# Kernel optimization log

Measured on AMD Instinct MI355X. Metric: run time of the kernel, lower is better.

The kernel has to match this reference:

```python
import jax, jax.numpy as jnp
import numpy as np

B, T, D_MODEL, N_HEADS = 2, 2048, 1024, 16


def setup_inputs() -> dict:
    key = jax.random.key(0)
    ks = jax.random.split(key, 5)
    w_scale = 0.02
    return {
        "x": jax.random.normal(ks[0], (B, T, D_MODEL), jnp.float32),
        "Wq": jax.random.normal(ks[1], (D_MODEL, D_MODEL), jnp.float32) * w_scale,
        "Wk": jax.random.normal(ks[2], (D_MODEL, D_MODEL), jnp.float32) * w_scale,
        "Wv": jax.random.normal(ks[3], (D_MODEL, D_MODEL), jnp.float32) * w_scale,
        "Wo": jax.random.normal(ks[4], (D_MODEL, D_MODEL), jnp.float32) * w_scale,
    }


def reference(x, Wq, Wk, Wv, Wo):
    Bv, Tv, _ = x.shape
    H = N_HEADS
    D = D_MODEL // H
    # Projections (torch nn.Linear: y = x @ W.T), split heads -> (B, H, T, D)
    q = (x @ Wq.T).reshape(Bv, Tv, H, D).transpose(0, 2, 1, 3)
    k = (x @ Wk.T).reshape(Bv, Tv, H, D).transpose(0, 2, 1, 3)
    v = (x @ Wv.T).reshape(Bv, Tv, H, D).transpose(0, 2, 1, 3)

    scale = jnp.sqrt(jnp.asarray(D, jnp.float32))
    scores = jnp.einsum("bhqd,bhkd->bhqk", q, k) / scale  # (B, H, T, T)

    # ALiBi bias: -|i-j| * slope_h, future positions masked to -inf (causal)
    slopes = jnp.asarray(
        [2.0 ** (-8.0 * h / H) for h in range(1, H + 1)], jnp.float32
    )
    pos = jnp.arange(Tv)
    dist = jnp.abs(pos[None, :] - pos[:, None]).astype(jnp.float32)  # (T, T)
    bias = -dist[None, :, :] * slopes[:, None, None]                 # (H, T, T)
    causal_mask = jnp.triu(jnp.ones((Tv, Tv), dtype=bool), 1)
    bias = jnp.where(causal_mask[None, :, :], -jnp.inf, bias)
    scores = scores + bias[None]  # (B, H, T, T)

    attn = jax.nn.softmax(scores, axis=-1)
    out = jnp.einsum("bhqk,bhkd->bhqd", attn, v)
    out = out.transpose(0, 2, 1, 3).reshape(Bv, Tv, D_MODEL)
    return out @ Wo.T
```

## Files before the change

kernel.cpp:

```cpp
#include <hip/hip_runtime.h>


#define DEV __device__ __forceinline__

typedef __attribute__((ext_vector_type(8))) short short8;
typedef __attribute__((ext_vector_type(4))) float f32x4;
typedef __attribute__((ext_vector_type(4))) unsigned short ushort4v;

DEV unsigned short f2bf(float f) {
  unsigned u = __builtin_bit_cast(unsigned, f);
  u += 0x7fffu + ((u >> 16) & 1u);
  return (unsigned short)(u >> 16);
}

DEV void gl2lds16(const void* g, void* l) {
  __builtin_amdgcn_global_load_lds(
      (const __attribute__((address_space(1))) void*)g,
      (__attribute__((address_space(3))) void*)l, 16, 0, 0);
}

__global__ __launch_bounds__(256) void cvt_all(
    const float* __restrict__ x, const float* __restrict__ wq,
    const float* __restrict__ wk, const float* __restrict__ wv,
    const float* __restrict__ wo, unsigned short* __restrict__ xb,
    unsigned short* __restrict__ wqb, unsigned short* __restrict__ wkb,
    unsigned short* __restrict__ wvb, unsigned short* __restrict__ wob) {
  int b = blockIdx.x;
  const float* s;
  unsigned short* d;
  int off;
  if (b < 4096)      { s = x;  d = xb;  off = b; }
  else if (b < 5120) { s = wq; d = wqb; off = b - 4096; }
  else if (b < 6144) { s = wk; d = wkb; off = b - 5120; }
  else if (b < 7168) { s = wv; d = wvb; off = b - 6144; }
  else               { s = wo; d = wob; off = b - 7168; }
  int i = (off * 256 + threadIdx.x) * 4;
  float4 v = *(const float4*)(s + i);
  ushort4v o = {f2bf(v.x), f2bf(v.y), f2bf(v.z), f2bf(v.w)};
  *(ushort4v*)(d + i) = o;
}

__global__ __launch_bounds__(256, 2) void gemm_qkv(
    const unsigned short* __restrict__ A, const unsigned short* __restrict__ Wq,
    const unsigned short* __restrict__ Wk, const unsigned short* __restrict__ Wv,
    unsigned short* __restrict__ Qo, unsigned short* __restrict__ Ko,
    unsigned short* __restrict__ Vo) {
  constexpr int K = 1024;
  __shared__ alignas(16) unsigned short Al[128 * 32];
  __shared__ alignas(16) unsigned short Bl[128 * 32];
  const int t = threadIdx.x;
  const int l = t & 63, l15 = l & 15, l4 = l >> 4;
  const int wm = ((t >> 6) & 1) * 64, wn = (t >> 7) * 64;
  const int wsel = blockIdx.x >> 3;
  const int n0 = (blockIdx.x & 7) * 128;
  const int m0 = blockIdx.y * 128;
  const unsigned short* Bm = (wsel == 0) ? Wq : ((wsel == 1) ? Wk : Wv);

  f32x4 zero4 = {0.f, 0.f, 0.f, 0.f};
  f32x4 acc[4][4];
#pragma unroll
  for (int i = 0; i < 4; i++)
#pragma unroll
    for (int j = 0; j < 4; j++) acc[i][j] = zero4;

  const int row0 = t >> 2, seg = (t & 3) * 8;
  const unsigned short* Ag0 = A + (m0 + row0) * K + seg;
  const unsigned short* Ag1 = A + (m0 + row0 + 64) * K + seg;
  const unsigned short* Bg0 = Bm + (n0 + row0) * K + seg;
  const unsigned short* Bg1 = Bm + (n0 + row0 + 64) * K + seg;

  for (int k0 = 0; k0 < K; k0 += 32) {
    gl2lds16(Ag0 + k0, &Al[t * 8]);
    gl2lds16(Ag1 + k0, &Al[2048 + t * 8]);
    gl2lds16(Bg0 + k0, &Bl[t * 8]);
    gl2lds16(Bg1 + k0, &Bl[2048 + t * 8]);
    __syncthreads();
    short8 af[4], bf8[4];
#pragma unroll
    for (int mi = 0; mi < 4; mi++)
      af[mi] = *(const short8*)&Al[(wm + mi * 16 + l15) * 32 + l4 * 8];
#pragma unroll
    for (int ni = 0; ni < 4; ni++)
      bf8[ni] = *(const short8*)&Bl[(wn + ni * 16 + l15) * 32 + l4 * 8];
#pragma unroll
    for (int mi = 0; mi < 4; mi++)
#pragma unroll
      for (int ni = 0; ni < 4; ni++)
        acc[mi][ni] = __builtin_amdgcn_mfma_f32_16x16x32_bf16(
            af[mi], bf8[ni], acc[mi][ni], 0, 0, 0);
    __syncthreads();
  }

  unsigned short* D = (wsel == 0) ? Qo : ((wsel == 1) ? Ko : Vo);
  const float scale = (wsel == 0) ? 0.18033688011112042f : 1.0f;
#pragma unroll
  for (int mi = 0; mi < 4; mi++)
#pragma unroll
    for (int r = 0; r < 4; r++) {
      int m = m0 + wm + mi * 16 + l4 * 4 + r;
      int b = m >> 11, tt = m & 2047;
#pragma unroll
      for (int ni = 0; ni < 4; ni++) {
        int n = n0 + wn + ni * 16 + l15;
        int z = b * 16 + (n >> 6), d = n & 63;
        float v = acc[mi][ni][r] * scale;
        int idx = (wsel == 2) ? ((z * 64 + d) * 2048 + tt)
                              : ((z * 2048 + tt) * 64 + d);
        D[idx] = f2bf(v);
      }
    }
}

__global__ __launch_bounds__(256, 2) void gemm_o(
    const unsigned short* __restrict__ A, const unsigned short* __restrict__ Bm,
    float* __restrict__ C) {
  constexpr int K = 1024;
  __shared__ alignas(16) unsigned short Al[128 * 32];
  __shared__ alignas(16) unsigned short Bl[128 * 32];
  const int t = threadIdx.x;
  const int l = t & 63, l15 = l & 15, l4 = l >> 4;
  const int wm = ((t >> 6) & 1) * 64, wn = (t >> 7) * 64;
  const int m0 = blockIdx.y * 128, n0 = blockIdx.x * 128;

  f32x4 zero4 = {0.f, 0.f, 0.f, 0.f};
  f32x4 acc[4][4];
#pragma unroll
  for (int i = 0; i < 4; i++)
#pragma unroll
    for (int j = 0; j < 4; j++) acc[i][j] = zero4;

  const int row0 = t >> 2, seg = (t & 3) * 8;
  const unsigned short* Ag0 = A + (m0 + row0) * K + seg;
  const unsigned short* Ag1 = A + (m0 + row0 + 64) * K + seg;
  const unsigned short* Bg0 = Bm + (n0 + row0) * K + seg;
  const unsigned short* Bg1 = Bm + (n0 + row0 + 64) * K + seg;

  for (int k0 = 0; k0 < K; k0 += 32) {
    gl2lds16(Ag0 + k0, &Al[t * 8]);
    gl2lds16(Ag1 + k0, &Al[2048 + t * 8]);
    gl2lds16(Bg0 + k0, &Bl[t * 8]);
    gl2lds16(Bg1 + k0, &Bl[2048 + t * 8]);
    __syncthreads();
    short8 af[4], bf8[4];
#pragma unroll
    for (int mi = 0; mi < 4; mi++)
      af[mi] = *(const short8*)&Al[(wm + mi * 16 + l15) * 32 + l4 * 8];
#pragma unroll
    for (int ni = 0; ni < 4; ni++)
      bf8[ni] = *(const short8*)&Bl[(wn + ni * 16 + l15) * 32 + l4 * 8];
#pragma unroll
    for (int mi = 0; mi < 4; mi++)
#pragma unroll
      for (int ni = 0; ni < 4; ni++)
        acc[mi][ni] = __builtin_amdgcn_mfma_f32_16x16x32_bf16(
            af[mi], bf8[ni], acc[mi][ni], 0, 0, 0);
    __syncthreads();
  }
#pragma unroll
  for (int mi = 0; mi < 4; mi++)
#pragma unroll
    for (int r = 0; r < 4; r++) {
      int m = m0 + wm + mi * 16 + l4 * 4 + r;
      float* cp = C + m * 1024 + n0 + wn + l15;
#pragma unroll
      for (int ni = 0; ni < 4; ni++) cp[ni * 16] = acc[mi][ni][r];
    }
}

__global__ __launch_bounds__(256, 3) void flash_alibi(
    const unsigned short* __restrict__ Q, const unsigned short* __restrict__ Kb,
    const unsigned short* __restrict__ Vt, unsigned short* __restrict__ O) {
  __shared__ alignas(16) unsigned short Kl[2 * 4096];
  __shared__ alignas(16) unsigned short Vl[2 * 4096];
  __shared__ alignas(16) unsigned short Pl[4 * 2304];
  const int t = threadIdx.x, w = t >> 6, l = t & 63, l15 = l & 15, l4 = l >> 4;
  const int g = blockIdx.x;
  const int qt = (g < 256) ? (15 - (g >> 5)) : ((g - 256) >> 5);
  const int z = g & 31;
  const int q0 = qt * 128, h = z & 15;
  const float slope2 = exp2f(-0.5f * (float)(h + 1)) * 1.4426950408889634f;
  const int qrow = q0 + w * 32;

  short8 aq[2][2];
#pragma unroll
  for (int mi = 0; mi < 2; mi++)
#pragma unroll
    for (int ks = 0; ks < 2; ks++)
      aq[mi][ks] = *(const short8*)&Q[(z * 2048 + qrow + mi * 16 + l15) * 64 +
                                      ks * 32 + l4 * 8];

  f32x4 binit[2];
#pragma unroll
  for (int mi = 0; mi < 2; mi++)
#pragma unroll
    for (int r = 0; r < 4; r++)
      binit[mi][r] =
          -(slope2 * (float)(qrow + mi * 16 + l4 * 4 + r) + 10.0f);

  f32x4 zero4 = {0.f, 0.f, 0.f, 0.f};
  f32x4 o[2][4];
  float lsum[2][4];
#pragma unroll
  for (int mi = 0; mi < 2; mi++)
#pragma unroll
    for (int j = 0; j < 4; j++) {
      o[mi][j] = zero4;
      lsum[mi][j] = 0.f;
    }

  const int row0 = t >> 2, seg8 = (t & 3) * 8;
  const int kvtiles = 2 * qt + 2;

#define ISSUE_LOADS(KV0, BUF)                                                \
  {                                                                          \
    unsigned short* Kd = &Kl[(BUF) * 4096];                                  \
    unsigned short* Vd = &Vl[(BUF) * 4096];                                  \
    gl2lds16(&Kb[(z * 2048 + (KV0) + row0) * 64 + seg8], &Kd[t * 8]);        \
    gl2lds16(&Kb[(z * 2048 + (KV0) + row0) * 64 + 32 + seg8],                \
             &Kd[2048 + t * 8]);                                             \
    gl2lds16(&Vt[(z * 64 + row0) * 2048 + (KV0) + seg8], &Vd[t * 8]);        \
    gl2lds16(&Vt[(z * 64 + row0) * 2048 + (KV0) + 32 + seg8],                \
             &Vd[2048 + t * 8]);                                             \
  }

  ISSUE_LOADS(0, 0)

  for (int it = 0; it < kvtiles; ++it) {
    __syncthreads();
    const int kv0 = it * 64;
    if (it + 1 < kvtiles) ISSUE_LOADS((it + 1) * 64, (it + 1) & 1)
    if (kv0 > qrow + 31) continue;
    const unsigned short* Kc = &Kl[(it & 1) * 4096];
    const unsigned short* Vc = &Vl[(it & 1) * 4096];

    f32x4 s[2][4];
#pragma unroll
    for (int mi = 0; mi < 2; mi++)
#pragma unroll
      for (int ni = 0; ni < 4; ni++) s[mi][ni] = binit[mi];
#pragma unroll
    for (int ks = 0; ks < 2; ks++) {
      short8 bk[4];
#pragma unroll
      for (int ni = 0; ni < 4; ni++)
        bk[ni] = *(const short8*)&Kc[(ks * 64 + ni * 16 + l15) * 32 + l4 * 8];
#pragma unroll
      for (int mi = 0; mi < 2; mi++)
#pragma unroll
        for (int ni = 0; ni < 4; ni++)
          s[mi][ni] = __builtin_amdgcn_mfma_f32_16x16x32_bf16(
              aq[mi][ks], bk[ni], s[mi][ni], 0, 0, 0);
    }

    const bool needMask = (kv0 + 63 > qrow);
    float jf[4];
#pragma unroll
    for (int ni = 0; ni < 4; ni++) jf[ni] = (float)(kv0 + ni * 16 + l15);

#pragma unroll
    for (int mi = 0; mi < 2; mi++)
#pragma unroll
      for (int r = 0; r < 4; r++) {
        float ps[4];
#pragma unroll
        for (int ni = 0; ni < 4; ni++)
          ps[ni] =
              __builtin_amdgcn_exp2f(fmaf(slope2, jf[ni], s[mi][ni][r]));
        if (needMask) {
          int qi = qrow + mi * 16 + l4 * 4 + r;
#pragma unroll
          for (int ni = 0; ni < 4; ni++)
            if (kv0 + ni * 16 + l15 > qi) ps[ni] = 0.f;
        }
        lsum[mi][r] += (ps[0] + ps[1]) + (ps[2] + ps[3]);
        int row = mi * 16 + l4 * 4 + r;
        unsigned short* pp = &Pl[w * 2304 + row * 72 + (l15 & 7)];
#pragma unroll
        for (int ni = 0; ni < 4; ni++)
          pp[((ni * 2 + (l15 >> 3)) ^ l4) * 8] = f2bf(ps[ni]);
      }

    asm volatile("s_waitcnt lgkmcnt(0)" ::: "memory");

    const int rsw = (l15 >> 2) & 3;
#pragma unroll
    for (int ks = 0; ks < 2; ks++) {
      short8 pf[2], vf[4];
#pragma unroll
      for (int mi = 0; mi < 2; mi++)
        pf[mi] = *(const short8*)&Pl[w * 2304 + (mi * 16 + l15) * 72 +
                                     ((ks * 4 + l4) ^ rsw) * 8];
#pragma unroll
      for (int nd = 0; nd < 4; nd++)
        vf[nd] = *(const short8*)&Vc[(ks * 64 + nd * 16 + l15) * 32 + l4 * 8];
#pragma unroll
      for (int mi = 0; mi < 2; mi++)
#pragma unroll
        for (int nd = 0; nd < 4; nd++)
          o[mi][nd] = __builtin_amdgcn_mfma_f32_16x16x32_bf16(
              pf[mi], vf[nd], o[mi][nd], 0, 0, 0);
    }
  }
#undef ISSUE_LOADS

  const int bq = z >> 4, hh = z & 15;
#pragma unroll
  for (int mi = 0; mi < 2; mi++)
#pragma unroll
    for (int r = 0; r < 4; r++) {
      float lv = lsum[mi][r];
#pragma unroll
      for (int off = 1; off < 16; off <<= 1) lv += __shfl_xor(lv, off);
      float inv = 1.0f / lv;
      int tg = qrow + mi * 16 + l4 * 4 + r;
      unsigned short* op = &O[(bq * 2048 + tg) * 1024 + hh * 64 + l15];
#pragma unroll
      for (int nd = 0; nd < 4; nd++) op[nd * 16] = f2bf(o[mi][nd][r] * inv);
    }
}

extern "C" void kernel_launch(void* const* d_in, const int* in_sizes, int n_in,
                              void* d_out, int out_size, void* d_ws,
                              size_t ws_size, hipStream_t stream) {
  const float* x = (const float*)d_in[0];
  const float* Wq = (const float*)d_in[1];
  const float* Wk = (const float*)d_in[2];
  const float* Wv = (const float*)d_in[3];
  const float* Wo = (const float*)d_in[4];

  char* p = (char*)d_ws;
  unsigned short* xb = (unsigned short*)p;  p += 4096 * 1024 * 2;
  unsigned short* wqb = (unsigned short*)p; p += 1024 * 1024 * 2;
  unsigned short* wkb = (unsigned short*)p; p += 1024 * 1024 * 2;
  unsigned short* wvb = (unsigned short*)p; p += 1024 * 1024 * 2;
  unsigned short* wob = (unsigned short*)p; p += 1024 * 1024 * 2;
  unsigned short* Qb = (unsigned short*)p;  p += 32 * 2048 * 64 * 2;
  unsigned short* Kbf = (unsigned short*)p; p += 32 * 2048 * 64 * 2;
  unsigned short* Vtb = (unsigned short*)p; p += 32 * 2048 * 64 * 2;
  unsigned short* Ob = (unsigned short*)p;  p += 4096 * 1024 * 2;

  cvt_all<<<8192, 256, 0, stream>>>(x, Wq, Wk, Wv, Wo, xb, wqb, wkb, wvb, wob);
  gemm_qkv<<<dim3(24, 32), 256, 0, stream>>>(xb, wqb, wkb, wvb, Qb, Kbf, Vtb);
  flash_alibi<<<512, 256, 0, stream>>>(Qb, Kbf, Vtb, Ob);
  gemm_o<<<dim3(8, 32), 256, 0, stream>>>(Ob, wob, (float*)d_out);
}
```

Baseline: 201.7 us.

## Split attention KV range across two blocks, add combine pass, retile output GEMM

The flash attention kernel now splits each query tile's KV range into two halves handled by separate blocks. Each block writes an unnormalized bf16 partial output and its row sums, and a new combine kernel adds the halves and normalizes. Because there is no running max, the two halves can be summed directly. The V transpose in the QKV GEMM is staged through shared memory so that global stores become coalesced 16-byte writes, and the output GEMM uses 128x64 tiles to double its block count. This is meant to improve load balance and occupancy on a part with many CUs, at the cost of an extra launch, extra intermediate traffic, and bf16 rounding of the partial sums.

Result: faster. 178.0 us (-11.7%).

```diff
diff --git a/kernel.cpp b/kernel.cpp
--- a/kernel.cpp
+++ b/kernel.cpp
@@ -11,6 +11,10 @@
   unsigned u = __builtin_bit_cast(unsigned, f);
   u += 0x7fffu + ((u >> 16) & 1u);
   return (unsigned short)(u >> 16);
+}
+DEV float bf2f(unsigned short u) {
+  unsigned x = ((unsigned)u) << 16;
+  return __builtin_bit_cast(float, x);
 }
 
 DEV void gl2lds16(const void* g, void* l) {
@@ -46,8 +50,9 @@
     unsigned short* __restrict__ Qo, unsigned short* __restrict__ Ko,
     unsigned short* __restrict__ Vo) {
   constexpr int K = 1024;
-  __shared__ alignas(16) unsigned short Al[128 * 32];
-  __shared__ alignas(16) unsigned short Bl[128 * 32];
+  __shared__ alignas(16) unsigned short Sm[18432];
+  unsigned short* Al = Sm;
+  unsigned short* Bl = Sm + 4096;
   const int t = threadIdx.x;
   const int l = t & 63, l15 = l & 15, l4 = l >> 4;
   const int wm = ((t >> 6) & 1) * 64, wn = (t >> 7) * 64;
@@ -91,24 +96,46 @@
     __syncthreads();
   }
 
-  unsigned short* D = (wsel == 0) ? Qo : ((wsel == 1) ? Ko : Vo);
-  const float scale = (wsel == 0) ? 0.18033688011112042f : 1.0f;
-#pragma unroll
-  for (int mi = 0; mi < 4; mi++)
-#pragma unroll
-    for (int r = 0; r < 4; r++) {
-      int m = m0 + wm + mi * 16 + l4 * 4 + r;
-      int b = m >> 11, tt = m & 2047;
-#pragma unroll
-      for (int ni = 0; ni < 4; ni++) {
-        int n = n0 + wn + ni * 16 + l15;
-        int z = b * 16 + (n >> 6), d = n & 63;
-        float v = acc[mi][ni][r] * scale;
-        int idx = (wsel == 2) ? ((z * 64 + d) * 2048 + tt)
-                              : ((z * 2048 + tt) * 64 + d);
-        D[idx] = f2bf(v);
+  if (wsel != 2) {
+    unsigned short* D = (wsel == 0) ? Qo : Ko;
+    const float scale = (wsel == 0) ? 0.18033688011112042f : 1.0f;
+#pragma unroll
+    for (int mi = 0; mi < 4; mi++)
+#pragma unroll
+      for (int r = 0; r < 4; r++) {
+        int m = m0 + wm + mi * 16 + l4 * 4 + r;
+        int b = m >> 11, tt = m & 2047;
+#pragma unroll
+        for (int ni = 0; ni < 4; ni++) {
+          int n = n0 + wn + ni * 16 + l15;
+          int z = b * 16 + (n >> 6), d = n & 63;
+          D[(z * 2048 + tt) * 64 + d] = f2bf(acc[mi][ni][r] * scale);
+        }
       }
-    }
+  } else {
+    unsigned short* Tr = Sm + (t >> 6) * 4608;
+#pragma unroll
+    for (int mi = 0; mi < 4; mi++)
+#pragma unroll
+      for (int r = 0; r < 4; r++) {
+        int tl = mi * 16 + l4 * 4 + r;
+#pragma unroll
+        for (int ni = 0; ni < 4; ni++)
+          Tr[(ni * 16 + l15) * 72 + tl] = f2bf(acc[mi][ni][r]);
+      }
+    __syncthreads();
+    const int bb = m0 >> 11, tbase = m0 & 2047;
+#pragma unroll
+    for (int it2 = 0; it2 < 8; it2++) {
+      int idx = it2 * 256 + t;
+      int row = idx >> 4, c = idx & 15;
+      int zh = row >> 6, dd = row & 63;
+      int wsrc = zh * 2 + (c >> 3);
+      short8 v = *(const short8*)&Sm[wsrc * 4608 + dd * 72 + (c & 7) * 8];
+      int zg = bb * 16 + (n0 >> 6) + zh;
+      *(short8*)&Vo[(zg * 64 + dd) * 2048 + tbase + c * 8] = v;
+    }
+  }
 }
 
 __global__ __launch_bounds__(256, 2) void gemm_o(
@@ -116,44 +143,42 @@
     float* __restrict__ C) {
   constexpr int K = 1024;
   __shared__ alignas(16) unsigned short Al[128 * 32];
-  __shared__ alignas(16) unsigned short Bl[128 * 32];
+  __shared__ alignas(16) unsigned short Bl[64 * 32];
   const int t = threadIdx.x;
   const int l = t & 63, l15 = l & 15, l4 = l >> 4;
-  const int wm = ((t >> 6) & 1) * 64, wn = (t >> 7) * 64;
-  const int m0 = blockIdx.y * 128, n0 = blockIdx.x * 128;
+  const int wm = ((t >> 6) & 1) * 64, wn = (t >> 7) * 32;
+  const int m0 = blockIdx.y * 128, n0 = blockIdx.x * 64;
 
   f32x4 zero4 = {0.f, 0.f, 0.f, 0.f};
-  f32x4 acc[4][4];
+  f32x4 acc[4][2];
 #pragma unroll
   for (int i = 0; i < 4; i++)
 #pragma unroll
-    for (int j = 0; j < 4; j++) acc[i][j] = zero4;
+    for (int j = 0; j < 2; j++) acc[i][j] = zero4;
 
   const int row0 = t >> 2, seg = (t & 3) * 8;
   const unsigned short* Ag0 = A + (m0 + row0) * K + seg;
   const unsigned short* Ag1 = A + (m0 + row0 + 64) * K + seg;
   const unsigned short* Bg0 = Bm + (n0 + row0) * K + seg;
-  const unsigned short* Bg1 = Bm + (n0 + row0 + 64) * K + seg;
 
   for (int k0 = 0; k0 < K; k0 += 32) {
     gl2lds16(Ag0 + k0, &Al[t * 8]);
     gl2lds16(Ag1 + k0, &Al[2048 + t * 8]);
     gl2lds16(Bg0 + k0, &Bl[t * 8]);
-    gl2lds16(Bg1 + k0, &Bl[2048 + t * 8]);
-    __syncthreads();
-    short8 af[4], bf8[4];
+    __syncthreads();
+    short8 af[4], bf2[2];
 #pragma unroll
     for (int mi = 0; mi < 4; mi++)
       af[mi] = *(const short8*)&Al[(wm + mi * 16 + l15) * 32 + l4 * 8];
 #pragma unroll
-    for (int ni = 0; ni < 4; ni++)
-      bf8[ni] = *(const short8*)&Bl[(wn + ni * 16 + l15) * 32 + l4 * 8];
-#pragma unroll
-    for (int mi = 0; mi < 4; mi++)
-#pragma unroll
-      for (int ni = 0; ni < 4; ni++)
+    for (int ni = 0; ni < 2; ni++)
+      bf2[ni] = *(const short8*)&Bl[(wn + ni * 16 + l15) * 32 + l4 * 8];
+#pragma unroll
+    for (int mi = 0; mi < 4; mi++)
+#pragma unroll
+      for (int ni = 0; ni < 2; ni++)
         acc[mi][ni] = __builtin_amdgcn_mfma_f32_16x16x32_bf16(
-            af[mi], bf8[ni], acc[mi][ni], 0, 0, 0);
+            af[mi], bf2[ni], acc[mi][ni], 0, 0, 0);
     __syncthreads();
   }
 #pragma unroll
@@ -162,21 +187,23 @@
     for (int r = 0; r < 4; r++) {
       int m = m0 + wm + mi * 16 + l4 * 4 + r;
       float* cp = C + m * 1024 + n0 + wn + l15;
-#pragma unroll
-      for (int ni = 0; ni < 4; ni++) cp[ni * 16] = acc[mi][ni][r];
+      cp[0] = acc[mi][0][r];
+      cp[16] = acc[mi][1][r];
     }
 }
 
 __global__ __launch_bounds__(256, 3) void flash_alibi(
     const unsigned short* __restrict__ Q, const unsigned short* __restrict__ Kb,
-    const unsigned short* __restrict__ Vt, unsigned short* __restrict__ O) {
+    const unsigned short* __restrict__ Vt, unsigned short* __restrict__ O0,
+    unsigned short* __restrict__ O1, float* __restrict__ L0,
+    float* __restrict__ L1) {
   __shared__ alignas(16) unsigned short Kl[2 * 4096];
   __shared__ alignas(16) unsigned short Vl[2 * 4096];
   __shared__ alignas(16) unsigned short Pl[4 * 2304];
   const int t = threadIdx.x, w = t >> 6, l = t & 63, l15 = l & 15, l4 = l >> 4;
   const int g = blockIdx.x;
-  const int qt = (g < 256) ? (15 - (g >> 5)) : ((g - 256) >> 5);
-  const int z = g & 31;
+  const int qt = 15 - (g >> 6);
+  const int z = (g & 63) >> 1, s = g & 1;
   const int q0 = qt * 128, h = z & 15;
   const float slope2 = exp2f(-0.5f * (float)(h + 1)) * 1.4426950408889634f;
   const int qrow = q0 + w * 32;
@@ -194,8 +221,7 @@
   for (int mi = 0; mi < 2; mi++)
 #pragma unroll
     for (int r = 0; r < 4; r++)
-      binit[mi][r] =
-          -(slope2 * (float)(qrow + mi * 16 + l4 * 4 + r) + 10.0f);
+      binit[mi][r] = -(slope2 * (float)(qrow + mi * 16 + l4 * 4 + r) + 10.0f);
 
   f32x4 zero4 = {0.f, 0.f, 0.f, 0.f};
   f32x4 o[2][4];
@@ -209,7 +235,8 @@
     }
 
   const int row0 = t >> 2, seg8 = (t & 3) * 8;
-  const int kvtiles = 2 * qt + 2;
+  const int it0 = s ? (qt + 1) : 0;
+  const int nt = qt + 1;
 
 #define ISSUE_LOADS(KV0, BUF)                                                \
   {                                                                          \
@@ -223,21 +250,21 @@
              &Vd[2048 + t * 8]);                                             \
   }
 
-  ISSUE_LOADS(0, 0)
-
-  for (int it = 0; it < kvtiles; ++it) {
-    __syncthreads();
-    const int kv0 = it * 64;
-    if (it + 1 < kvtiles) ISSUE_LOADS((it + 1) * 64, (it + 1) & 1)
+  ISSUE_LOADS(it0 * 64, 0)
+
+  for (int ii = 0; ii < nt; ++ii) {
+    __syncthreads();
+    const int kv0 = (it0 + ii) * 64;
+    if (ii + 1 < nt) ISSUE_LOADS(kv0 + 64, (ii + 1) & 1)
     if (kv0 > qrow + 31) continue;
-    const unsigned short* Kc = &Kl[(it & 1) * 4096];
-    const unsigned short* Vc = &Vl[(it & 1) * 4096];
-
-    f32x4 s[2][4];
+    const unsigned short* Kc = &Kl[(ii & 1) * 4096];
+    const unsigned short* Vc = &Vl[(ii & 1) * 4096];
+
+    f32x4 sc[2][4];
 #pragma unroll
     for (int mi = 0; mi < 2; mi++)
 #pragma unroll
-      for (int ni = 0; ni < 4; ni++) s[mi][ni] = binit[mi];
+      for (int ni = 0; ni < 4; ni++) sc[mi][ni] = binit[mi];
 #pragma unroll
     for (int ks = 0; ks < 2; ks++) {
       short8 bk[4];
@@ -248,8 +275,8 @@
       for (int mi = 0; mi < 2; mi++)
 #pragma unroll
         for (int ni = 0; ni < 4; ni++)
-          s[mi][ni] = __builtin_amdgcn_mfma_f32_16x16x32_bf16(
-              aq[mi][ks], bk[ni], s[mi][ni], 0, 0, 0);
+          sc[mi][ni] = __builtin_amdgcn_mfma_f32_16x16x32_bf16(
+              aq[mi][ks], bk[ni], sc[mi][ni], 0, 0, 0);
     }
 
     const bool needMask = (kv0 + 63 > qrow);
@@ -264,8 +291,7 @@
         float ps[4];
 #pragma unroll
         for (int ni = 0; ni < 4; ni++)
-          ps[ni] =
-              __builtin_amdgcn_exp2f(fmaf(slope2, jf[ni], s[mi][ni][r]));
+          ps[ni] = __builtin_amdgcn_exp2f(fmaf(slope2, jf[ni], sc[mi][ni][r]));
         if (needMask) {
           int qi = qrow + mi * 16 + l4 * 4 + r;
 #pragma unroll
@@ -303,7 +329,8 @@
   }
 #undef ISSUE_LOADS
 
-  const int bq = z >> 4, hh = z & 15;
+  unsigned short* Op = s ? O1 : O0;
+  float* Lp = s ? L1 : L0;
 #pragma unroll
   for (int mi = 0; mi < 2; mi++)
 #pragma unroll
@@ -311,12 +338,32 @@
       float lv = lsum[mi][r];
 #pragma unroll
       for (int off = 1; off < 16; off <<= 1) lv += __shfl_xor(lv, off);
-      float inv = 1.0f / lv;
       int tg = qrow + mi * 16 + l4 * 4 + r;
-      unsigned short* op = &O[(bq * 2048 + tg) * 1024 + hh * 64 + l15];
-#pragma unroll
-      for (int nd = 0; nd < 4; nd++) op[nd * 16] = f2bf(o[mi][nd][r] * inv);
-    }
+      if (l15 == 0) Lp[z * 2048 + tg] = lv;
+      unsigned short* op = &Op[(z * 2048 + tg) * 64 + l15];
+#pragma unroll
+      for (int nd = 0; nd < 4; nd++) op[nd * 16] = f2bf(o[mi][nd][r]);
+    }
+}
+
+__global__ __launch_bounds__(256) void combine(
+    const unsigned short* __restrict__ O0, const unsigned short* __restrict__ O1,
+    const float* __restrict__ L0, const float* __restrict__ L1,
+    unsigned short* __restrict__ Ob) {
+  int idx = (blockIdx.x * 256 + threadIdx.x) * 8;
+  int z = idx >> 17, rem = idx & 131071;
+  int tt = rem >> 6, d = rem & 63;
+  short8 a = *(const short8*)(O0 + idx);
+  short8 b = *(const short8*)(O1 + idx);
+  float inv = 1.0f / (L0[z * 2048 + tt] + L1[z * 2048 + tt]);
+  short8 o;
+#pragma unroll
+  for (int j = 0; j < 8; j++) {
+    float v = (bf2f((unsigned short)a[j]) + bf2f((unsigned short)b[j])) * inv;
+    o[j] = (short)f2bf(v);
+  }
+  int bq = z >> 4, h = z & 15;
+  *(short8*)(Ob + (bq * 2048 + tt) * 1024 + h * 64 + d) = o;
 }
 
 extern "C" void kernel_launch(void* const* d_in, const int* in_sizes, int n_in,
@@ -337,10 +384,15 @@
   unsigned short* Qb = (unsigned short*)p;  p += 32 * 2048 * 64 * 2;
   unsigned short* Kbf = (unsigned short*)p; p += 32 * 2048 * 64 * 2;
   unsigned short* Vtb = (unsigned short*)p; p += 32 * 2048 * 64 * 2;
-  unsigned short* Ob = (unsigned short*)p;  p += 4096 * 1024 * 2;
+  unsigned short* O1 = (unsigned short*)p;  p += 32 * 2048 * 64 * 2;
+  float* L0 = (float*)p;                    p += 32 * 2048 * 4;
+  float* L1 = (float*)p;                    p += 32 * 2048 * 4;
+  unsigned short* O0 = xb;
+  unsigned short* Ob = Qb;
 
   cvt_all<<<8192, 256, 0, stream>>>(x, Wq, Wk, Wv, Wo, xb, wqb, wkb, wvb, wob);
   gemm_qkv<<<dim3(24, 32), 256, 0, stream>>>(xb, wqb, wkb, wvb, Qb, Kbf, Vtb);
-  flash_alibi<<<512, 256, 0, stream>>>(Qb, Kbf, Vtb, Ob);
-  gemm_o<<<dim3(8, 32), 256, 0, stream>>>(Ob, wob, (float*)d_out);
-}
+  flash_alibi<<<1024, 256, 0, stream>>>(Qb, Kbf, Vtb, O0, O1, L0, L1);
+  combine<<<2048, 256, 0, stream>>>(O0, O1, L0, L1, Ob);
+  gemm_o<<<dim3(16, 32), 256, 0, stream>>>(Ob, wob, (float*)d_out);
+}
```
